# Kernel tuning notes

Measured on AMD Instinct MI355X. Metric: run time of the kernel, lower is better.

The kernel has to match this reference:

```python
import jax, jax.numpy as jnp
import numpy as np

MD_S = 1
MD_R = 16
EVAL_STEPS = 7
INV_T = 100.0
EPS = 1e-6

B, C, S = 16, 512, 4096  # batch, channels, flattened spatial


def setup_inputs() -> dict:
    key = jax.random.key(0)
    k1, k2 = jax.random.split(key)
    x = jax.random.uniform(k1, (B, C, S), dtype=jnp.float32)  # non-negative input for NMF
    bases = jax.random.uniform(k2, (B * MD_S, S, MD_R), dtype=jnp.float32)
    # F.normalize(bases, dim=1)
    bases = bases / (jnp.linalg.norm(bases, axis=1, keepdims=True) + 1e-12)
    return {"x": x, "bases": bases}


def _nmf_step(xm, bases, coef):
    # xm: (BS, D, N), bases: (BS, D, R), coef: (BS, N, R)
    # multiplicative update for coef
    num = jnp.einsum('bdn,bdr->bnr', xm, bases)
    den = jnp.einsum('bnr,brs->bns', coef, jnp.einsum('bdr,bds->brs', bases, bases))
    coef = coef * num / (den + EPS)
    # multiplicative update for bases
    num = jnp.einsum('bdn,bnr->bdr', xm, coef)
    den = jnp.einsum('bdr,brs->bds', bases, jnp.einsum('bnr,bns->brs', coef, coef))
    bases = bases * num / (den + EPS)
    return bases, coef


def _local_inference(xm, bases):
    # coef init: softmax(inv_t * x^T bases)
    coef = jax.nn.softmax(INV_T * jnp.einsum('bdn,bdr->bnr', xm, bases), axis=-1)

    def body(carry, _):
        b, c = _nmf_step(xm, carry[0], carry[1])
        return (b, c), None

    (bases, coef), _ = jax.lax.scan(body, (bases, coef), None, length=EVAL_STEPS)
    return bases, coef


def reference(x, bases):
    Bb, Cc, Ss = x.shape
    D = Ss
    N = Cc // MD_S
    xm = x.reshape(Bb * MD_S, N, D).transpose(0, 2, 1)  # (BS, D, N)

    bases_i, coef_i = jax.lax.stop_gradient(_local_inference(xm, bases))

    # compute_coef (differentiable in the original module)
    num = jnp.einsum('bdn,bdr->bnr', xm, bases_i)
    den = jnp.einsum('bnr,brs->bns', coef_i, jnp.einsum('bdr,bds->brs', bases_i, bases_i))
    coef = coef_i * num / (den + EPS)

    # x_rec = bases @ coef^T -> (BS, D, N) -> transpose -> (B, C, S)
    out = jnp.einsum('bdr,bnr->bdn', bases_i, coef)
    out = out.transpose(0, 2, 1).reshape(Bb, Cc, Ss)
    return out
```

## Files before the change

kernel.cpp:

```cpp
#include <hip/hip_runtime.h>

#define EPS 1e-6f

template <int CTRL>
__device__ __forceinline__ float dpp_add(float v) {
  int moved = __builtin_amdgcn_update_dpp(0, __float_as_int(v), CTRL, 0xF, 0xF, false);
  return v + __int_as_float(moved);
}

__global__ __launch_bounds__(256) void kernelT(
    const float* __restrict__ bin, float* __restrict__ bT)
{
  __shared__ float t[256][17];
  const int tid = threadIdx.x;
  const int ds = blockIdx.x;
  const int b = blockIdx.y;
  const float4* __restrict__ src =
      (const float4*)(bin + ((size_t)(b * 4096 + ds * 256 + tid)) * 16);
  float4 a0 = src[0], a1 = src[1], a2 = src[2], a3 = src[3];
  t[tid][0] = a0.x;  t[tid][1] = a0.y;  t[tid][2] = a0.z;  t[tid][3] = a0.w;
  t[tid][4] = a1.x;  t[tid][5] = a1.y;  t[tid][6] = a1.z;  t[tid][7] = a1.w;
  t[tid][8] = a2.x;  t[tid][9] = a2.y;  t[tid][10] = a2.z; t[tid][11] = a2.w;
  t[tid][12] = a3.x; t[tid][13] = a3.y; t[tid][14] = a3.z; t[tid][15] = a3.w;
  __syncthreads();
  const int r = tid >> 4;
  const int i0 = (tid & 15) * 16;
  float* __restrict__ dst = bT + ((size_t)(b * 16 + r)) * 4096 + ds * 256 + i0;
#pragma unroll
  for (int j = 0; j < 16; ++j) dst[j] = t[i0 + j][r];
}

__global__ __launch_bounds__(256, 3) void kernelA(
    const float* __restrict__ x, const float* __restrict__ bT,
    float* __restrict__ Ppart, float* __restrict__ CtC)
{
  const int tid = threadIdx.x;
  const int grp = blockIdx.x;
  const int b = blockIdx.y;
  const int h = blockIdx.z;
  if (h == 0 && grp == 0) CtC[b * 256 + tid] = 0.0f;
  const int w = tid >> 6;
  const int lane = tid & 63;
  const int n0 = grp * 16 + w * 4;
  const float* __restrict__ xp =
      x + ((size_t)(b * 512 + n0)) * 4096 + h * 2048 + lane * 4;
  const float* __restrict__ bp =
      bT + ((size_t)(b * 16)) * 4096 + h * 2048 + lane * 4;

  float acc[4][16];
#pragma unroll
  for (int i = 0; i < 4; ++i)
#pragma unroll
    for (int r = 0; r < 16; ++r) acc[i][r] = 0.0f;

  float4 xv[4], xn[4];
#pragma unroll
  for (int i = 0; i < 4; ++i) xv[i] = *(const float4*)(xp + (size_t)i * 4096);

  for (int c = 0; c < 8; ++c) {
    if (c < 7) {
#pragma unroll
      for (int i = 0; i < 4; ++i)
        xn[i] = *(const float4*)(xp + (size_t)i * 4096 + (c + 1) * 256);
    }
#pragma unroll
    for (int rg = 0; rg < 4; ++rg) {
      float4 bq[4];
#pragma unroll
      for (int j = 0; j < 4; ++j)
        bq[j] = *(const float4*)(bp + (size_t)(rg * 4 + j) * 4096 + c * 256);
#pragma unroll
      for (int i = 0; i < 4; ++i) {
#pragma unroll
        for (int j = 0; j < 4; ++j) {
          float s = acc[i][rg * 4 + j];
          s = fmaf(xv[i].x, bq[j].x, s);
          s = fmaf(xv[i].y, bq[j].y, s);
          s = fmaf(xv[i].z, bq[j].z, s);
          s = fmaf(xv[i].w, bq[j].w, s);
          acc[i][rg * 4 + j] = s;
        }
      }
    }
#pragma unroll
    for (int i = 0; i < 4; ++i) xv[i] = xn[i];
  }

#pragma unroll
  for (int i = 0; i < 4; ++i)
#pragma unroll
    for (int r = 0; r < 16; ++r) {
      float v = acc[i][r];
      v = dpp_add<0x121>(v);
      v = dpp_add<0x122>(v);
      v = dpp_add<0x124>(v);
      v = dpp_add<0x128>(v);
      v += __shfl_xor(v, 16, 64);
      v += __shfl_xor(v, 32, 64);
      acc[i][r] = v;
    }

  if (lane == 0) {
    float* __restrict__ pp =
        Ppart + (((size_t)(h * 16 + b)) * 512 + n0) * 16;
#pragma unroll
    for (int i = 0; i < 4; ++i) {
#pragma unroll
      for (int q = 0; q < 4; ++q)
        *(float4*)(pp + i * 16 + q * 4) =
            make_float4(acc[i][q * 4], acc[i][q * 4 + 1], acc[i][q * 4 + 2], acc[i][q * 4 + 3]);
    }
  }
}

__global__ __launch_bounds__(256) void kernelSM(
    const float* __restrict__ Ppart, float* __restrict__ coef)
{
  const int gid = blockIdx.x * 256 + threadIdx.x;
  const int b = gid >> 9, n = gid & 511;
  const float* __restrict__ p0 = Ppart + (((size_t)b) * 512 + n) * 16;
  const float* __restrict__ p1 = Ppart + (((size_t)(16 + b)) * 512 + n) * 16;
  float p[16];
#pragma unroll
  for (int r = 0; r < 16; ++r) p[r] = p0[r] + p1[r];
  float m = p[0];
#pragma unroll
  for (int r = 1; r < 16; ++r) m = fmaxf(m, p[r]);
  float e[16];
  float s = 0.0f;
#pragma unroll
  for (int r = 0; r < 16; ++r) { e[r] = __expf(100.0f * (p[r] - m)); s += e[r]; }
  float inv = 1.0f / s;
  float* __restrict__ crow = coef + (((size_t)b) * 512 + n) * 16;
#pragma unroll
  for (int r = 0; r < 16; ++r) crow[r] = e[r] * inv;
}

__global__ __launch_bounds__(256) void kernelGram(
    const float* __restrict__ M, float* __restrict__ out, int L)
{
  __shared__ __align__(16) float sm[256 * 20];
  __shared__ __align__(16) float part[4 * 272];
  const int tid = threadIdx.x;
  const int b = blockIdx.y;
  const int sl = blockIdx.x;
  const float4* __restrict__ src = (const float4*)(M + ((size_t)b * L + (size_t)sl * 256) * 16);
#pragma unroll
  for (int k = 0; k < 4; ++k) {
    int idx = k * 256 + tid;
    int row = idx >> 2, q = idx & 3;
    *(float4*)(&sm[row * 20 + q * 4]) = src[idx];
  }
  __syncthreads();
  const int rq = tid & 3;
  const int s = (tid >> 2) & 15;
  const int g = tid >> 6;
  float a0 = 0.f, a1 = 0.f, a2 = 0.f, a3 = 0.f;
#pragma unroll 4
  for (int l = g * 64; l < g * 64 + 64; ++l) {
    float4 bv = *(const float4*)(&sm[l * 20 + rq * 4]);
    float cs = sm[l * 20 + s];
    a0 = fmaf(cs, bv.x, a0);
    a1 = fmaf(cs, bv.y, a1);
    a2 = fmaf(cs, bv.z, a2);
    a3 = fmaf(cs, bv.w, a3);
  }
  *(float4*)(&part[g * 272 + s * 16 + rq * 4]) = make_float4(a0, a1, a2, a3);
  __syncthreads();
  float v = part[0 * 272 + tid] + part[1 * 272 + tid] + part[2 * 272 + tid] + part[3 * 272 + tid];
  atomicAdd(out + b * 256 + tid, v);
}

__global__ __launch_bounds__(256) void kernelCU(
    float* __restrict__ coef, const float* __restrict__ Ppart,
    const float* __restrict__ BtBr, float* __restrict__ BtBz,
    float* __restrict__ CtCadd)
{
  __shared__ __align__(16) float sm[256 * 20 + 4 * 272];
  const int tid = threadIdx.x;
  BtBz[blockIdx.x * 128 + (tid & 127)] = 0.0f;
  const int b = blockIdx.x >> 1;
  const int n = ((blockIdx.x & 1) << 8) + tid;
  float* __restrict__ crow = coef + ((size_t)(b * 512 + n)) * 16;
  const float* __restrict__ p0 = Ppart + (((size_t)b) * 512 + n) * 16;
  const float* __restrict__ p1 = Ppart + (((size_t)(16 + b)) * 512 + n) * 16;
  const float* __restrict__ btb = BtBr + b * 256;
  float cv[16], den[16];
#pragma unroll
  for (int r = 0; r < 16; ++r) cv[r] = crow[r];
#pragma unroll
  for (int r = 0; r < 16; ++r) den[r] = 0.f;
#pragma unroll
  for (int s2 = 0; s2 < 16; ++s2) {
    const float bs = cv[s2];
#pragma unroll
    for (int r = 0; r < 16; ++r) den[r] = fmaf(bs, btb[s2 * 16 + r], den[r]);
  }
#pragma unroll
  for (int r = 0; r < 16; ++r) {
    float cn = cv[r] * (p0[r] + p1[r]) / (den[r] + EPS);
    crow[r] = cn;
    sm[tid * 20 + r] = cn;
  }
  __syncthreads();
  const int rq = tid & 3;
  const int s = (tid >> 2) & 15;
  const int g = tid >> 6;
  float a0 = 0.f, a1 = 0.f, a2 = 0.f, a3 = 0.f;
#pragma unroll 4
  for (int l = g * 64; l < g * 64 + 64; ++l) {
    float4 bv = *(const float4*)(&sm[l * 20 + rq * 4]);
    float cs = sm[l * 20 + s];
    a0 = fmaf(cs, bv.x, a0);
    a1 = fmaf(cs, bv.y, a1);
    a2 = fmaf(cs, bv.z, a2);
    a3 = fmaf(cs, bv.w, a3);
  }
  float* part = sm + 5120;
  *(float4*)(&part[g * 272 + s * 16 + rq * 4]) = make_float4(a0, a1, a2, a3);
  __syncthreads();
  float v = part[0 * 272 + tid] + part[1 * 272 + tid] + part[2 * 272 + tid] + part[3 * 272 + tid];
  atomicAdd(CtCadd + b * 256 + tid, v);
}

__global__ __launch_bounds__(256) void kernelBacc(
    const float* __restrict__ x, const float* __restrict__ coef,
    float* __restrict__ qpart)
{
  const int tid = threadIdx.x;
  const int dt = blockIdx.x, ns = blockIdx.y, b = blockIdx.z;
  const int d = dt * 256 + tid;
  const float* __restrict__ xp = x + ((size_t)(b * 512 + ns * 128)) * 4096 + d;
  const float* __restrict__ cp = coef + ((size_t)(b * 512 + ns * 128)) * 16;
  float acc[16];
#pragma unroll
  for (int r = 0; r < 16; ++r) acc[r] = 0.f;
#pragma unroll 4
  for (int n = 0; n < 128; ++n) {
    const float xv = xp[(size_t)n * 4096];
    const float* __restrict__ crow = cp + n * 16;
#pragma unroll
    for (int r = 0; r < 16; ++r) acc[r] = fmaf(xv, crow[r], acc[r]);
  }
  float* __restrict__ qp = qpart + (((size_t)(ns * 16 + b)) * 4096 + d) * 16;
#pragma unroll
  for (int q = 0; q < 4; ++q)
    *(float4*)(qp + q * 4) = make_float4(acc[q * 4], acc[q * 4 + 1], acc[q * 4 + 2], acc[q * 4 + 3]);
}

__global__ __launch_bounds__(256) void kernelBfin(
    const float* __restrict__ qpart, float* __restrict__ bases,
    float* __restrict__ bT,
    const float* __restrict__ CtC, float* __restrict__ BtBadd)
{
  __shared__ __align__(16) float sm[256 * 20 + 4 * 272];
  const int tid = threadIdx.x;
  const int dt = blockIdx.x, b = blockIdx.y;
  const int d = dt * 256 + tid;
  float acc[16];
#pragma unroll
  for (int r = 0; r < 16; ++r) acc[r] = 0.f;
#pragma unroll
  for (int ns = 0; ns < 4; ++ns) {
    const float* __restrict__ qp = qpart + (((size_t)(ns * 16 + b)) * 4096 + d) * 16;
#pragma unroll
    for (int q = 0; q < 4; ++q) {
      float4 v = *(const float4*)(qp + q * 4);
      acc[q * 4 + 0] += v.x; acc[q * 4 + 1] += v.y; acc[q * 4 + 2] += v.z; acc[q * 4 + 3] += v.w;
    }
  }
  float* __restrict__ brow = bases + ((size_t)(b * 4096 + d)) * 16;
  float bv[16];
#pragma unroll
  for (int r = 0; r < 16; ++r) bv[r] = brow[r];
  const float* __restrict__ ctc = CtC + b * 256;
  float den[16];
#pragma unroll
  for (int r = 0; r < 16; ++r) den[r] = 0.f;
#pragma unroll
  for (int s2 = 0; s2 < 16; ++s2) {
    const float bs = bv[s2];
#pragma unroll
    for (int r = 0; r < 16; ++r) den[r] = fmaf(bs, ctc[s2 * 16 + r], den[r]);
  }
  float* __restrict__ btr = bT + ((size_t)(b * 16)) * 4096 + d;
#pragma unroll
  for (int r = 0; r < 16; ++r) {
    float bn = bv[r] * acc[r] / (den[r] + EPS);
    brow[r] = bn;
    btr[(size_t)r * 4096] = bn;
    sm[tid * 20 + r] = bn;
  }
  __syncthreads();
  const int rq = tid & 3;
  const int s = (tid >> 2) & 15;
  const int g = tid >> 6;
  float a0 = 0.f, a1 = 0.f, a2 = 0.f, a3 = 0.f;
#pragma unroll 4
  for (int l = g * 64; l < g * 64 + 64; ++l) {
    float4 bq = *(const float4*)(&sm[l * 20 + rq * 4]);
    float cs = sm[l * 20 + s];
    a0 = fmaf(cs, bq.x, a0);
    a1 = fmaf(cs, bq.y, a1);
    a2 = fmaf(cs, bq.z, a2);
    a3 = fmaf(cs, bq.w, a3);
  }
  float* part = sm + 5120;
  *(float4*)(&part[g * 272 + s * 16 + rq * 4]) = make_float4(a0, a1, a2, a3);
  __syncthreads();
  float v = part[0 * 272 + tid] + part[1 * 272 + tid] + part[2 * 272 + tid] + part[3 * 272 + tid];
  atomicAdd(BtBadd + b * 256 + tid, v);
}

__global__ __launch_bounds__(256) void kernelOut(
    const float* __restrict__ bases, const float* __restrict__ coef,
    float* __restrict__ out)
{
  const int tid = threadIdx.x;
  const int dt = blockIdx.x, ns = blockIdx.y, b = blockIdx.z;
  const int d0 = dt * 1024 + tid * 4;
  float bv[4][16];
#pragma unroll
  for (int k = 0; k < 4; ++k) {
    const float* __restrict__ brow = bases + ((size_t)(b * 4096 + d0 + k)) * 16;
#pragma unroll
    for (int r = 0; r < 16; ++r) bv[k][r] = brow[r];
  }
  const float* __restrict__ cp = coef + ((size_t)(b * 512 + ns * 32)) * 16;
  float* __restrict__ op = out + ((size_t)(b * 512 + ns * 32)) * 4096 + d0;
#pragma unroll 4
  for (int n = 0; n < 32; ++n) {
    const float* __restrict__ crow = cp + n * 16;
    float v[4];
#pragma unroll
    for (int k = 0; k < 4; ++k) {
      float s = 0.f;
#pragma unroll
      for (int r = 0; r < 16; ++r) s = fmaf(bv[k][r], crow[r], s);
      v[k] = s;
    }
    *(float4*)(op + (size_t)n * 4096) = make_float4(v[0], v[1], v[2], v[3]);
  }
}

extern "C" void kernel_launch(void* const* d_in, const int* in_sizes, int n_in,
                              void* d_out, int out_size, void* d_ws, size_t ws_size,
                              hipStream_t stream) {
  const float* x = (const float*)d_in[0];
  const float* bases_in = (const float*)d_in[1];
  float* out = (float*)d_out;
  float* ws = (float*)d_ws;

  float* bases = ws;
  float* coef  = bases + 1048576;
  float* Ppart = coef + 131072;
  float* btb0  = Ppart + 262144;
  float* btb1  = btb0 + 4096;
  float* ctc   = btb1 + 4096;
  float* bT    = ctc + 4096;
  float* qpart = bT + 1048576;
  float* btb[2] = {btb0, btb1};

  hipMemsetAsync(btb0, 0, 4096 * sizeof(float), stream);
  hipMemcpyAsync(bases, bases_in, 1048576 * sizeof(float),
                 hipMemcpyDeviceToDevice, stream);
  kernelT<<<dim3(16, 16), 256, 0, stream>>>(bases_in, bT);

  kernelA<<<dim3(32, 16, 2), 256, 0, stream>>>(x, bT, Ppart, ctc);
  kernelSM<<<32, 256, 0, stream>>>(Ppart, coef);
  kernelGram<<<dim3(16, 16), 256, 0, stream>>>(bases, btb0, 4096);

  for (int t = 0; t < 7; ++t) {
    if (t > 0) kernelA<<<dim3(32, 16, 2), 256, 0, stream>>>(x, bT, Ppart, ctc);
    kernelCU<<<32, 256, 0, stream>>>(coef, Ppart, btb[t & 1], btb[(t + 1) & 1], ctc);
    kernelBacc<<<dim3(16, 4, 16), 256, 0, stream>>>(x, coef, qpart);
    kernelBfin<<<dim3(16, 16), 256, 0, stream>>>(qpart, bases, bT, ctc, btb[(t + 1) & 1]);
  }

  kernelA<<<dim3(32, 16, 2), 256, 0, stream>>>(x, bT, Ppart, ctc);
  kernelCU<<<32, 256, 0, stream>>>(coef, Ppart, btb[1], btb[0], ctc);
  kernelOut<<<dim3(4, 16, 16), 256, 0, stream>>>(bases, coef, out);
}
```

Baseline: 971.3 us.

## Halve kernelA rows per warp, double grid, and software-pipeline x and bases loads

kernelA now handles 2 rows of x per warp instead of 4 and launches twice as many blocks, with the occupancy hint raised from 3 to 4 blocks per CU. x loads are prefetched two chunks ahead and bases loads are double-buffered one row-group ahead, so memory latency overlaps the FMAs. The aim is more waves in flight and better latency hiding for this memory-bound x·bases product. In exchange, each bases chunk is reused across fewer x rows, so total bases reads from cache double.

```diff
diff --git a/kernel.cpp b/kernel.cpp
--- a/kernel.cpp
+++ b/kernel.cpp
@@ -30,7 +30,7 @@
   for (int j = 0; j < 16; ++j) dst[j] = t[i0 + j][r];
 }
 
-__global__ __launch_bounds__(256, 3) void kernelA(
+__global__ __launch_bounds__(256, 4) void kernelA(
     const float* __restrict__ x, const float* __restrict__ bT,
     float* __restrict__ Ppart, float* __restrict__ CtC)
 {
@@ -41,53 +41,70 @@
   if (h == 0 && grp == 0) CtC[b * 256 + tid] = 0.0f;
   const int w = tid >> 6;
   const int lane = tid & 63;
-  const int n0 = grp * 16 + w * 4;
+  const int n0 = grp * 8 + w * 2;
   const float* __restrict__ xp =
       x + ((size_t)(b * 512 + n0)) * 4096 + h * 2048 + lane * 4;
   const float* __restrict__ bp =
       bT + ((size_t)(b * 16)) * 4096 + h * 2048 + lane * 4;
 
-  float acc[4][16];
-#pragma unroll
-  for (int i = 0; i < 4; ++i)
+  float acc[2][16];
+#pragma unroll
+  for (int i = 0; i < 2; ++i)
 #pragma unroll
     for (int r = 0; r < 16; ++r) acc[i][r] = 0.0f;
 
-  float4 xv[4], xn[4];
-#pragma unroll
-  for (int i = 0; i < 4; ++i) xv[i] = *(const float4*)(xp + (size_t)i * 4096);
+  const float4 z4 = make_float4(0.f, 0.f, 0.f, 0.f);
+  float4 xv[2], xn1[2], xn2[2];
+  xn2[0] = z4; xn2[1] = z4;
+  xv[0]  = *(const float4*)(xp);
+  xv[1]  = *(const float4*)(xp + 4096);
+  xn1[0] = *(const float4*)(xp + 256);
+  xn1[1] = *(const float4*)(xp + 4096 + 256);
+
+  float4 bq[2][4];
+#pragma unroll
+  for (int j = 0; j < 4; ++j)
+    bq[0][j] = *(const float4*)(bp + (size_t)j * 4096);
+  bq[1][0] = z4; bq[1][1] = z4; bq[1][2] = z4; bq[1][3] = z4;
 
   for (int c = 0; c < 8; ++c) {
-    if (c < 7) {
-#pragma unroll
-      for (int i = 0; i < 4; ++i)
-        xn[i] = *(const float4*)(xp + (size_t)i * 4096 + (c + 1) * 256);
+    if (c < 6) {
+      xn2[0] = *(const float4*)(xp + (size_t)(c + 2) * 256);
+      xn2[1] = *(const float4*)(xp + 4096 + (size_t)(c + 2) * 256);
     }
 #pragma unroll
     for (int rg = 0; rg < 4; ++rg) {
-      float4 bq[4];
-#pragma unroll
-      for (int j = 0; j < 4; ++j)
-        bq[j] = *(const float4*)(bp + (size_t)(rg * 4 + j) * 4096 + c * 256);
-#pragma unroll
-      for (int i = 0; i < 4; ++i) {
+      const int cur = rg & 1, nxt = cur ^ 1;
+      if (rg < 3) {
+#pragma unroll
+        for (int j = 0; j < 4; ++j)
+          bq[nxt][j] =
+              *(const float4*)(bp + (size_t)((rg + 1) * 4 + j) * 4096 + c * 256);
+      } else if (c < 7) {
+#pragma unroll
+        for (int j = 0; j < 4; ++j)
+          bq[nxt][j] =
+              *(const float4*)(bp + (size_t)j * 4096 + (c + 1) * 256);
+      }
+#pragma unroll
+      for (int i = 0; i < 2; ++i) {
 #pragma unroll
         for (int j = 0; j < 4; ++j) {
           float s = acc[i][rg * 4 + j];
-          s = fmaf(xv[i].x, bq[j].x, s);
-          s = fmaf(xv[i].y, bq[j].y, s);
-          s = fmaf(xv[i].z, bq[j].z, s);
-          s = fmaf(xv[i].w, bq[j].w, s);
+          s = fmaf(xv[i].x, bq[cur][j].x, s);
+          s = fmaf(xv[i].y, bq[cur][j].y, s);
+          s = fmaf(xv[i].z, bq[cur][j].z, s);
+          s = fmaf(xv[i].w, bq[cur][j].w, s);
           acc[i][rg * 4 + j] = s;
         }
       }
     }
-#pragma unroll
-    for (int i = 0; i < 4; ++i) xv[i] = xn[i];
-  }
-
-#pragma unroll
-  for (int i = 0; i < 4; ++i)
+    xv[0] = xn1[0]; xv[1] = xn1[1];
+    xn1[0] = xn2[0]; xn1[1] = xn2[1];
+  }
+
+#pragma unroll
+  for (int i = 0; i < 2; ++i)
 #pragma unroll
     for (int r = 0; r < 16; ++r) {
       float v = acc[i][r];
@@ -104,7 +121,7 @@
     float* __restrict__ pp =
         Ppart + (((size_t)(h * 16 + b)) * 512 + n0) * 16;
 #pragma unroll
-    for (int i = 0; i < 4; ++i) {
+    for (int i = 0; i < 2; ++i) {
 #pragma unroll
       for (int q = 0; q < 4; ++q)
         *(float4*)(pp + i * 16 + q * 4) =
@@ -366,18 +383,18 @@
                  hipMemcpyDeviceToDevice, stream);
   kernelT<<<dim3(16, 16), 256, 0, stream>>>(bases_in, bT);
 
-  kernelA<<<dim3(32, 16, 2), 256, 0, stream>>>(x, bT, Ppart, ctc);
+  kernelA<<<dim3(64, 16, 2), 256, 0, stream>>>(x, bT, Ppart, ctc);
   kernelSM<<<32, 256, 0, stream>>>(Ppart, coef);
   kernelGram<<<dim3(16, 16), 256, 0, stream>>>(bases, btb0, 4096);
 
   for (int t = 0; t < 7; ++t) {
-    if (t > 0) kernelA<<<dim3(32, 16, 2), 256, 0, stream>>>(x, bT, Ppart, ctc);
+    if (t > 0) kernelA<<<dim3(64, 16, 2), 256, 0, stream>>>(x, bT, Ppart, ctc);
     kernelCU<<<32, 256, 0, stream>>>(coef, Ppart, btb[t & 1], btb[(t + 1) & 1], ctc);
     kernelBacc<<<dim3(16, 4, 16), 256, 0, stream>>>(x, coef, qpart);
     kernelBfin<<<dim3(16, 16), 256, 0, stream>>>(qpart, bases, bT, ctc, btb[(t + 1) & 1]);
   }
 
-  kernelA<<<dim3(32, 16, 2), 256, 0, stream>>>(x, bT, Ppart, ctc);
+  kernelA<<<dim3(64, 16, 2), 256, 0, stream>>>(x, bT, Ppart, ctc);
   kernelCU<<<32, 256, 0, stream>>>(coef, Ppart, btb[1], btb[0], ctc);
   kernelOut<<<dim3(4, 16, 16), 256, 0, stream>>>(bases, coef, out);
 }
```

Result: slower. 1.160 ms (+19.5%).
